# Kernel optimization log

Hardware: AMD Instinct MI355X
Metric: run time of the kernel (lower is better)

Reference implementation:

```python
import jax, jax.numpy as jnp
import numpy as np

T, B, L, I, H = 1024, 1024, 10, 10, 10


def setup_inputs() -> dict:
    key = jax.random.key(0)
    ks = jax.random.split(key, 7)
    scale = 1.0 / np.sqrt(H)
    x = jax.random.normal(ks[0], (T, B, I), dtype=jnp.float32)
    hp = jax.random.normal(ks[1], (L, B, H), dtype=jnp.float32)
    cp = jax.random.normal(ks[2], (L, B, H), dtype=jnp.float32)
    # torch nn.LSTM params, uniform(-1/sqrt(H), 1/sqrt(H)); layer 0 input = I == H so all layers stack
    W_ih = jax.random.uniform(ks[3], (L, 4 * H, I), minval=-scale, maxval=scale, dtype=jnp.float32)
    W_hh = jax.random.uniform(ks[4], (L, 4 * H, H), minval=-scale, maxval=scale, dtype=jnp.float32)
    b_ih = jax.random.uniform(ks[5], (L, 4 * H), minval=-scale, maxval=scale, dtype=jnp.float32)
    b_hh = jax.random.uniform(ks[6], (L, 4 * H), minval=-scale, maxval=scale, dtype=jnp.float32)
    return {"x": x, "hp": hp, "cp": cp, "W_ih": W_ih, "W_hh": W_hh, "b_ih": b_ih, "b_hh": b_hh}


def _run_layer(inp, h0, c0, Wi, Wh, bi, bh):
    # precompute input projections for all timesteps: [T, B, 4H]
    xg = jnp.einsum('tbi,gi->tbg', inp, Wi) + bi + bh

    def step(carry, xg_t):
        h, c = carry
        g = xg_t + h @ Wh.T  # [B, 4H]; torch gate order: i, f, g, o
        i_g, f_g, g_g, o_g = jnp.split(g, 4, axis=-1)
        i_g = jax.nn.sigmoid(i_g)
        f_g = jax.nn.sigmoid(f_g)
        g_g = jnp.tanh(g_g)
        o_g = jax.nn.sigmoid(o_g)
        c = f_g * c + i_g * g_g
        h = o_g * jnp.tanh(c)
        return (h, c), h

    (hT, cT), ys = jax.lax.scan(step, (h0, c0), xg)
    return ys, hT, cT


def reference(x, hp, cp, W_ih, W_hh, b_ih, b_hh):
    out = x
    hns, cns = [], []
    for l in range(hp.shape[0]):  # fixed small layer stack
        out, hn, cn = _run_layer(out, hp[l], cp[l], W_ih[l], W_hh[l], b_ih[l], b_hh[l])
        hns.append(hn)
        cns.append(cn)
    return out, jnp.stack(hns), jnp.stack(cns)
```

## Files before the change

kernel.cpp:

```cpp
#include <hip/hip_runtime.h>

namespace {

constexpr int T = 1024;
constexpr int B = 1024;
constexpr int L = 10;
constexpr int H = 10;
constexpr int NTHREADS = 128;
constexpr int U = 4;
constexpr int NWIN = T / U;
constexpr int NINT = NWIN + L - 1;
constexpr int BH = B * H;
constexpr int WSLOT = 84;

using v2f = __attribute__((ext_vector_type(2))) float;

__device__ __forceinline__ v2f v2fma(v2f a, v2f b, v2f c) {
    return __builtin_elementwise_fma(a, b, c);
}
__device__ __forceinline__ void pin2(v2f& v) { asm volatile("" : "+v"(v)); }
__device__ __forceinline__ void pin1(float& v) { asm volatile("" : "+v"(v)); }

__device__ __forceinline__ float sigmoid_f(float x) {
    return __builtin_amdgcn_rcpf(1.0f + __expf(-x));
}
__device__ __forceinline__ float tanh_f(float x) {
    return 1.0f - 2.0f * __builtin_amdgcn_rcpf(1.0f + __expf(2.0f * x));
}

__global__
__attribute__((amdgpu_flat_work_group_size(NTHREADS, NTHREADS)))
__attribute__((amdgpu_waves_per_eu(1)))
void lstm_pipeline(const float* __restrict__ x,
                   const float* __restrict__ hp,
                   const float* __restrict__ cp,
                   const float* __restrict__ Wih,
                   const float* __restrict__ Whh,
                   const float* __restrict__ bih,
                   const float* __restrict__ bhh,
                   float* __restrict__ out,
                   float* __restrict__ hn,
                   float* __restrict__ cn)
{
    __shared__ __align__(16) float wlds[L * H * WSLOT];
    __shared__ __align__(16) float buf[L + 1][2][U][12];
    __shared__ __align__(16) float hbuf[L][12];

    const int tid = threadIdx.x;
    const int wv = tid >> 6, ln = tid & 63;
    int lidx;
    if (wv == 0) lidx = (ln < 60) ? ln : (ln - 10);
    else         lidx = (ln < 40) ? (60 + ln) : (90 + (ln - 40) % 10);
    const int l = lidx / 10;
    const int j = lidx % 10;
    const int b = blockIdx.x;
    const int boff = b * H + j;

    {
        float* slot = &wlds[lidx * WSLOT];
        #pragma unroll
        for (int g = 0; g < 4; ++g) {
            const int row = l * 4 * H + g * H + j;
            const float* wr = Wih + (size_t)row * H;
            const float* hr = Whh + (size_t)row * H;
            #pragma unroll
            for (int i = 0; i < H; ++i) slot[g * H + i] = wr[i];
            #pragma unroll
            for (int i = 0; i < H; ++i) slot[40 + g * H + i] = hr[i];
            slot[80 + g] = bih[row] + bhh[row];
        }
    }
    __syncthreads();

    v2f wi2[4][5], wh2[4][5];
    float bias[4];
    {
        const float* slot = &wlds[lidx * WSLOT];
        #pragma unroll
        for (int g = 0; g < 4; ++g) {
            #pragma unroll
            for (int p = 0; p < 5; ++p) {
                wi2[g][p] = *(const v2f*)&slot[g * H + 2 * p];
                wh2[g][p] = *(const v2f*)&slot[40 + g * H + 2 * p];
            }
            bias[g] = slot[80 + g];
        }
    }
    #pragma unroll
    for (int g = 0; g < 4; ++g) {
        #pragma unroll
        for (int p = 0; p < 5; ++p) { pin2(wi2[g][p]); pin2(wh2[g][p]); }
        pin1(bias[g]);
    }

    float h = hp[(l * B + b) * H + j];
    float c = cp[(l * B + b) * H + j];
    hbuf[l][j] = h;

    float xcur[U], xnext[U];
    if (lidx < 10) {
        #pragma unroll
        for (int u = 0; u < U; ++u) buf[0][1][u][j] = x[(size_t)u * BH + boff];
        #pragma unroll
        for (int u = 0; u < U; ++u) xcur[u] = x[(size_t)(U + u) * BH + boff];
    }
    __syncthreads();

    auto interval = [&](int k, int wp, int rp) {
        if (lidx < 10 && (k + 2) < NWIN) {
            #pragma unroll
            for (int u = 0; u < U; ++u)
                xnext[u] = x[(size_t)((k + 2) * U + u) * BH + boff];
        }
        const unsigned w = (unsigned)(k - l);
        if (w < (unsigned)NWIN) {
            float hv[U];
            #pragma unroll
            for (int u = 0; u < U; ++u) {
                float xin[10], hin[10];
                {
                    const float* xr = &buf[l][rp][u][0];
                    *(float4*)&xin[0] = *(const float4*)(xr);
                    *(float4*)&xin[4] = *(const float4*)(xr + 4);
                    *(float2*)&xin[8] = *(const float2*)(xr + 8);
                    const float* hr = &hbuf[l][0];
                    *(float4*)&hin[0] = *(const float4*)(hr);
                    *(float4*)&hin[4] = *(const float4*)(hr + 4);
                    *(float2*)&hin[8] = *(const float2*)(hr + 8);
                }
                v2f a0, a1, a2, a3;
                a0[0] = bias[0]; a0[1] = 0.0f;
                a1[0] = bias[1]; a1[1] = 0.0f;
                a2[0] = bias[2]; a2[1] = 0.0f;
                a3[0] = bias[3]; a3[1] = 0.0f;
                #pragma unroll
                for (int p = 0; p < 5; ++p) {
                    v2f xp; xp[0] = xin[2 * p]; xp[1] = xin[2 * p + 1];
                    a0 = v2fma(wi2[0][p], xp, a0);
                    a1 = v2fma(wi2[1][p], xp, a1);
                    a2 = v2fma(wi2[2][p], xp, a2);
                    a3 = v2fma(wi2[3][p], xp, a3);
                }
                #pragma unroll
                for (int p = 0; p < 5; ++p) {
                    v2f hh; hh[0] = hin[2 * p]; hh[1] = hin[2 * p + 1];
                    a0 = v2fma(wh2[0][p], hh, a0);
                    a1 = v2fma(wh2[1][p], hh, a1);
                    a2 = v2fma(wh2[2][p], hh, a2);
                    a3 = v2fma(wh2[3][p], hh, a3);
                }
                const float ig = sigmoid_f(a0[0] + a0[1]);
                const float fg = sigmoid_f(a1[0] + a1[1]);
                const float gg = tanh_f(a2[0] + a2[1]);
                const float og = sigmoid_f(a3[0] + a3[1]);
                c = fmaf(fg, c, ig * gg);
                h = og * tanh_f(c);

                hbuf[l][j] = h;
                buf[l + 1][wp][u][j] = h;
                hv[u] = h;
            }
            if (l == L - 1) {
                const int t0 = (int)w * U;
                #pragma unroll
                for (int u = 0; u < U; ++u)
                    out[(size_t)(t0 + u) * BH + boff] = hv[u];
            }
        }
        if (lidx < 10 && (k + 1) < NWIN) {
            #pragma unroll
            for (int u = 0; u < U; ++u) buf[0][wp][u][j] = xcur[u];
            #pragma unroll
            for (int u = 0; u < U; ++u) xcur[u] = xnext[u];
        }
        __syncthreads();
    };

    for (int kk = 0; kk < NINT + 1; kk += 2) {
        interval(kk, 0, 1);
        interval(kk + 1, 1, 0);
    }

    hn[(l * B + b) * H + j] = h;
    cn[(l * B + b) * H + j] = c;
}

}

extern "C" void kernel_launch(void* const* d_in, const int* in_sizes, int n_in,
                              void* d_out, int out_size, void* d_ws, size_t ws_size,
                              hipStream_t stream) {
    (void)in_sizes; (void)n_in; (void)d_ws; (void)ws_size; (void)out_size;
    const float* x   = (const float*)d_in[0];
    const float* hp  = (const float*)d_in[1];
    const float* cp  = (const float*)d_in[2];
    const float* Wih = (const float*)d_in[3];
    const float* Whh = (const float*)d_in[4];
    const float* bih = (const float*)d_in[5];
    const float* bhh = (const float*)d_in[6];

    float* out = (float*)d_out;
    float* hn  = out + (size_t)T * B * H;
    float* cn  = hn + (size_t)L * B * H;

    lstm_pipeline<<<dim3(B), dim3(NTHREADS), 0, stream>>>(
        x, hp, cp, Wih, Whh, bih, bhh, out, hn, cn);
}
```

Baseline: 502.6 us.

## Split each LSTM hidden unit's gates across two lanes with DPP exchange

Each hidden unit now runs on a pair of lanes, and each lane computes two of the four gates, so the block grows to 256 threads. Inputs and hidden states are stored duplicated, which lets packed v2f FMAs consume them directly, and the four gate activations are exchanged between paired lanes with a DPP swap. The input projection for all U steps is hoisted ahead of the serial recurrence, and the LDS weight staging is replaced by direct global loads. The aim is to halve the per-lane FMA and transcendental work on the critical serial path. The cost is more waves per block, duplicated LDS writes, and a cross-lane shuffle on every step.

New measurement: 638.7 us. 1.27x slower.

```diff
diff --git a/kernel.cpp b/kernel.cpp
--- a/kernel.cpp
+++ b/kernel.cpp
@@ -6,31 +6,30 @@
 constexpr int B = 1024;
 constexpr int L = 10;
 constexpr int H = 10;
-constexpr int NTHREADS = 128;
+constexpr int NTHREADS = 256;
 constexpr int U = 4;
 constexpr int NWIN = T / U;
 constexpr int NINT = NWIN + L - 1;
 constexpr int BH = B * H;
-constexpr int WSLOT = 84;
+constexpr int ROW = 24;
 
 using v2f = __attribute__((ext_vector_type(2))) float;
+using v4f = __attribute__((ext_vector_type(4))) float;
 
 __device__ __forceinline__ v2f v2fma(v2f a, v2f b, v2f c) {
     return __builtin_elementwise_fma(a, b, c);
 }
 __device__ __forceinline__ void pin2(v2f& v) { asm volatile("" : "+v"(v)); }
-__device__ __forceinline__ void pin1(float& v) { asm volatile("" : "+v"(v)); }
-
-__device__ __forceinline__ float sigmoid_f(float x) {
-    return __builtin_amdgcn_rcpf(1.0f + __expf(-x));
-}
-__device__ __forceinline__ float tanh_f(float x) {
-    return 1.0f - 2.0f * __builtin_amdgcn_rcpf(1.0f + __expf(2.0f * x));
-}
+__device__ __forceinline__ float rcp_f(float x) { return __builtin_amdgcn_rcpf(x); }
+__device__ __forceinline__ float dpp_swap1(float v) {
+    return __int_as_float(__builtin_amdgcn_mov_dpp(__float_as_int(v), 0xB1, 0xF, 0xF, true));
+}
+__device__ __forceinline__ v2f lo2(v4f q) { return __builtin_shufflevector(q, q, 0, 1); }
+__device__ __forceinline__ v2f hi2(v4f q) { return __builtin_shufflevector(q, q, 2, 3); }
 
 __global__
 __attribute__((amdgpu_flat_work_group_size(NTHREADS, NTHREADS)))
-__attribute__((amdgpu_waves_per_eu(1)))
+__attribute__((amdgpu_waves_per_eu(4)))
 void lstm_pipeline(const float* __restrict__ x,
                    const float* __restrict__ hp,
                    const float* __restrict__ cp,
@@ -42,136 +41,139 @@
                    float* __restrict__ hn,
                    float* __restrict__ cn)
 {
-    __shared__ __align__(16) float wlds[L * H * WSLOT];
-    __shared__ __align__(16) float buf[L + 1][2][U][12];
-    __shared__ __align__(16) float hbuf[L][12];
+    __shared__ __align__(16) float buf[2][U][L + 1][ROW];
+    __shared__ __align__(16) float hbuf[L][ROW];
 
     const int tid = threadIdx.x;
-    const int wv = tid >> 6, ln = tid & 63;
-    int lidx;
-    if (wv == 0) lidx = (ln < 60) ? ln : (ln - 10);
-    else         lidx = (ln < 40) ? (60 + ln) : (90 + (ln - 40) % 10);
-    const int l = lidx / 10;
-    const int j = lidx % 10;
+    const int wv = tid >> 6;
+    const int ln = tid & 63;
+    int q, l;
+    if (wv < 3) { q = (ln < 60) ? ln : (ln - 8); l = 3 * wv + q / 20; }
+    else        { q = ln % 20;  l = 9; }
+    const int j = (q % 20) >> 1;
+    const int p = q & 1;
     const int b = blockIdx.x;
     const int boff = b * H + j;
 
+    v2f wipk[10], whpk[10], biasv;
     {
-        float* slot = &wlds[lidx * WSLOT];
+        const int r0 = (l * 4 + 2 * p) * H + j;
+        const float* wi0 = Wih + (size_t)r0 * H;
+        const float* wh0 = Whh + (size_t)r0 * H;
         #pragma unroll
-        for (int g = 0; g < 4; ++g) {
-            const int row = l * 4 * H + g * H + j;
-            const float* wr = Wih + (size_t)row * H;
-            const float* hr = Whh + (size_t)row * H;
-            #pragma unroll
-            for (int i = 0; i < H; ++i) slot[g * H + i] = wr[i];
-            #pragma unroll
-            for (int i = 0; i < H; ++i) slot[40 + g * H + i] = hr[i];
-            slot[80 + g] = bih[row] + bhh[row];
-        }
-    }
-    __syncthreads();
-
-    v2f wi2[4][5], wh2[4][5];
-    float bias[4];
-    {
-        const float* slot = &wlds[lidx * WSLOT];
-        #pragma unroll
-        for (int g = 0; g < 4; ++g) {
-            #pragma unroll
-            for (int p = 0; p < 5; ++p) {
-                wi2[g][p] = *(const v2f*)&slot[g * H + 2 * p];
-                wh2[g][p] = *(const v2f*)&slot[40 + g * H + 2 * p];
-            }
-            bias[g] = slot[80 + g];
-        }
+        for (int i = 0; i < H; ++i) {
+            wipk[i][0] = wi0[i]; wipk[i][1] = wi0[H * H + i];
+            whpk[i][0] = wh0[i]; whpk[i][1] = wh0[H * H + i];
+        }
+        biasv[0] = bih[r0] + bhh[r0];
+        biasv[1] = bih[r0 + H] + bhh[r0 + H];
     }
     #pragma unroll
-    for (int g = 0; g < 4; ++g) {
-        #pragma unroll
-        for (int p = 0; p < 5; ++p) { pin2(wi2[g][p]); pin2(wh2[g][p]); }
-        pin1(bias[g]);
-    }
+    for (int i = 0; i < H; ++i) { pin2(wipk[i]); pin2(whpk[i]); }
+    pin2(biasv);
+    const float s0 = p ? 2.0f : -1.0f;
 
     float h = hp[(l * B + b) * H + j];
     float c = cp[(l * B + b) * H + j];
-    hbuf[l][j] = h;
-
-    float xcur[U], xnext[U];
-    if (lidx < 10) {
+    { v2f hh; hh[0] = h; hh[1] = h; *(v2f*)&hbuf[l][2 * j] = hh; }
+
+    const bool stager = (l == 0 && p == 0);
+    float xcur[U];
+    if (stager) {
         #pragma unroll
-        for (int u = 0; u < U; ++u) buf[0][1][u][j] = x[(size_t)u * BH + boff];
+        for (int u = 0; u < U; ++u) {
+            float xv = x[(size_t)u * BH + boff];
+            v2f xx; xx[0] = xv; xx[1] = xv;
+            *(v2f*)&buf[1][u][0][2 * j] = xx;
+        }
         #pragma unroll
         for (int u = 0; u < U; ++u) xcur[u] = x[(size_t)(U + u) * BH + boff];
     }
     __syncthreads();
 
     auto interval = [&](int k, int wp, int rp) {
-        if (lidx < 10 && (k + 2) < NWIN) {
-            #pragma unroll
-            for (int u = 0; u < U; ++u)
-                xnext[u] = x[(size_t)((k + 2) * U + u) * BH + boff];
-        }
         const unsigned w = (unsigned)(k - l);
         if (w < (unsigned)NWIN) {
+            v2f acc[U];
+            #pragma unroll
+            for (int u = 0; u < U; ++u) {
+                const float* xr = &buf[rp][u][l][0];
+                v4f q0 = *(const v4f*)(xr + 0);
+                v4f q1 = *(const v4f*)(xr + 4);
+                v4f q2 = *(const v4f*)(xr + 8);
+                v4f q3 = *(const v4f*)(xr + 12);
+                v4f q4 = *(const v4f*)(xr + 16);
+                v2f z; z[0] = 0.0f; z[1] = 0.0f;
+                v2f a  = v2fma(wipk[0], lo2(q0), biasv);
+                v2f a2 = v2fma(wipk[1], hi2(q0), z);
+                a  = v2fma(wipk[2], lo2(q1), a);
+                a2 = v2fma(wipk[3], hi2(q1), a2);
+                a  = v2fma(wipk[4], lo2(q2), a);
+                a2 = v2fma(wipk[5], hi2(q2), a2);
+                a  = v2fma(wipk[6], lo2(q3), a);
+                a2 = v2fma(wipk[7], hi2(q3), a2);
+                a  = v2fma(wipk[8], lo2(q4), a);
+                a2 = v2fma(wipk[9], hi2(q4), a2);
+                acc[u] = a + a2;
+            }
             float hv[U];
             #pragma unroll
             for (int u = 0; u < U; ++u) {
-                float xin[10], hin[10];
-                {
-                    const float* xr = &buf[l][rp][u][0];
-                    *(float4*)&xin[0] = *(const float4*)(xr);
-                    *(float4*)&xin[4] = *(const float4*)(xr + 4);
-                    *(float2*)&xin[8] = *(const float2*)(xr + 8);
-                    const float* hr = &hbuf[l][0];
-                    *(float4*)&hin[0] = *(const float4*)(hr);
-                    *(float4*)&hin[4] = *(const float4*)(hr + 4);
-                    *(float2*)&hin[8] = *(const float2*)(hr + 8);
-                }
-                v2f a0, a1, a2, a3;
-                a0[0] = bias[0]; a0[1] = 0.0f;
-                a1[0] = bias[1]; a1[1] = 0.0f;
-                a2[0] = bias[2]; a2[1] = 0.0f;
-                a3[0] = bias[3]; a3[1] = 0.0f;
-                #pragma unroll
-                for (int p = 0; p < 5; ++p) {
-                    v2f xp; xp[0] = xin[2 * p]; xp[1] = xin[2 * p + 1];
-                    a0 = v2fma(wi2[0][p], xp, a0);
-                    a1 = v2fma(wi2[1][p], xp, a1);
-                    a2 = v2fma(wi2[2][p], xp, a2);
-                    a3 = v2fma(wi2[3][p], xp, a3);
-                }
-                #pragma unroll
-                for (int p = 0; p < 5; ++p) {
-                    v2f hh; hh[0] = hin[2 * p]; hh[1] = hin[2 * p + 1];
-                    a0 = v2fma(wh2[0][p], hh, a0);
-                    a1 = v2fma(wh2[1][p], hh, a1);
-                    a2 = v2fma(wh2[2][p], hh, a2);
-                    a3 = v2fma(wh2[3][p], hh, a3);
-                }
-                const float ig = sigmoid_f(a0[0] + a0[1]);
-                const float fg = sigmoid_f(a1[0] + a1[1]);
-                const float gg = tanh_f(a2[0] + a2[1]);
-                const float og = sigmoid_f(a3[0] + a3[1]);
+                const float* hr = &hbuf[l][0];
+                v4f q0 = *(const v4f*)(hr + 0);
+                v4f q1 = *(const v4f*)(hr + 4);
+                v4f q2 = *(const v4f*)(hr + 8);
+                v4f q3 = *(const v4f*)(hr + 12);
+                v4f q4 = *(const v4f*)(hr + 16);
+                v2f z; z[0] = 0.0f; z[1] = 0.0f;
+                v2f a  = v2fma(whpk[0], lo2(q0), acc[u]);
+                v2f a2 = v2fma(whpk[1], hi2(q0), z);
+                a  = v2fma(whpk[2], lo2(q1), a);
+                a2 = v2fma(whpk[3], hi2(q1), a2);
+                a  = v2fma(whpk[4], lo2(q2), a);
+                a2 = v2fma(whpk[5], hi2(q2), a2);
+                a  = v2fma(whpk[6], lo2(q3), a);
+                a2 = v2fma(whpk[7], hi2(q3), a2);
+                a  = v2fma(whpk[8], lo2(q4), a);
+                a2 = v2fma(whpk[9], hi2(q4), a2);
+                v2f pre = a + a2;
+                const float e0 = __expf(pre[0] * s0);
+                const float e1 = __expf(-pre[1]);
+                const float r0 = rcp_f(1.0f + e0);
+                const float r1 = rcp_f(1.0f + e1);
+                const float x0 = dpp_swap1(r0);
+                const float x1 = dpp_swap1(r1);
+                const float ig = p ? x0 : r0;
+                const float fg = p ? x1 : r1;
+                const float og = p ? r1 : x1;
+                const float gs = p ? r0 : x0;
+                const float gg = fmaf(-2.0f, gs, 1.0f);
                 c = fmaf(fg, c, ig * gg);
-                h = og * tanh_f(c);
-
-                hbuf[l][j] = h;
-                buf[l + 1][wp][u][j] = h;
+                const float th = 1.0f - 2.0f * rcp_f(1.0f + __expf(2.0f * c));
+                h = og * th;
+                v2f hh; hh[0] = h; hh[1] = h;
+                *(v2f*)&hbuf[l][2 * j] = hh;
+                *(v2f*)&buf[wp][u][l + 1][2 * j] = hh;
                 hv[u] = h;
             }
-            if (l == L - 1) {
+            if (l == L - 1 && p == 0) {
                 const int t0 = (int)w * U;
                 #pragma unroll
                 for (int u = 0; u < U; ++u)
                     out[(size_t)(t0 + u) * BH + boff] = hv[u];
             }
         }
-        if (lidx < 10 && (k + 1) < NWIN) {
+        if (stager && (k + 1) < NWIN) {
             #pragma unroll
-            for (int u = 0; u < U; ++u) buf[0][wp][u][j] = xcur[u];
-            #pragma unroll
-            for (int u = 0; u < U; ++u) xcur[u] = xnext[u];
+            for (int u = 0; u < U; ++u) {
+                v2f xx; xx[0] = xcur[u]; xx[1] = xcur[u];
+                *(v2f*)&buf[wp][u][0][2 * j] = xx;
+            }
+            if ((k + 2) < NWIN) {
+                #pragma unroll
+                for (int u = 0; u < U; ++u)
+                    xcur[u] = x[(size_t)((k + 2) * U + u) * BH + boff];
+            }
         }
         __syncthreads();
     };
```

## Process two batch rows per block with gate-paired packed FMAs and hoisted input projections

Applied to the files above, without the earlier changes.

Each block now handles two batch rows, so every thread's register-resident weights are reused across both rows and the grid is halved. Weights are repacked so each packed FMA computes two gates at once with duplicated inputs stored in LDS. The input projection for all U substeps is hoisted ahead of the recurrent chain. The exp and rcp calls of the two rows are interleaved to expose instruction-level parallelism. This trades fewer blocks (512 on a 256-CU part) and doubled per-block serial work for more ILP and fewer redundant weight loads and syncs.

New measurement: 834.1 us. +66.0%, slower.

```diff
diff --git a/kernel.cpp b/kernel.cpp
--- a/kernel.cpp
+++ b/kernel.cpp
@@ -7,26 +7,23 @@
 constexpr int L = 10;
 constexpr int H = 10;
 constexpr int NTHREADS = 128;
+constexpr int NB = 2;
 constexpr int U = 4;
 constexpr int NWIN = T / U;
 constexpr int NINT = NWIN + L - 1;
 constexpr int BH = B * H;
-constexpr int WSLOT = 84;
+constexpr int ROWF = 20;
 
 using v2f = __attribute__((ext_vector_type(2))) float;
+using v4f = __attribute__((ext_vector_type(4))) float;
 
 __device__ __forceinline__ v2f v2fma(v2f a, v2f b, v2f c) {
     return __builtin_elementwise_fma(a, b, c);
 }
 __device__ __forceinline__ void pin2(v2f& v) { asm volatile("" : "+v"(v)); }
-__device__ __forceinline__ void pin1(float& v) { asm volatile("" : "+v"(v)); }
-
-__device__ __forceinline__ float sigmoid_f(float x) {
-    return __builtin_amdgcn_rcpf(1.0f + __expf(-x));
-}
-__device__ __forceinline__ float tanh_f(float x) {
-    return 1.0f - 2.0f * __builtin_amdgcn_rcpf(1.0f + __expf(2.0f * x));
-}
+__device__ __forceinline__ float rcp_f(float x) { return __builtin_amdgcn_rcpf(x); }
+__device__ __forceinline__ v2f lo2(v4f q) { return __builtin_shufflevector(q, q, 0, 1); }
+__device__ __forceinline__ v2f hi2(v4f q) { return __builtin_shufflevector(q, q, 2, 3); }
 
 __global__
 __attribute__((amdgpu_flat_work_group_size(NTHREADS, NTHREADS)))
@@ -42,134 +39,174 @@
                    float* __restrict__ hn,
                    float* __restrict__ cn)
 {
-    __shared__ __align__(16) float wlds[L * H * WSLOT];
-    __shared__ __align__(16) float buf[L + 1][2][U][12];
-    __shared__ __align__(16) float hbuf[L][12];
+    __shared__ __align__(16) float buf[NB][2][U][L + 1][ROWF];
 
     const int tid = threadIdx.x;
-    const int wv = tid >> 6, ln = tid & 63;
+    const int wv = tid >> 6;
+    const int ln = tid & 63;
     int lidx;
     if (wv == 0) lidx = (ln < 60) ? ln : (ln - 10);
     else         lidx = (ln < 40) ? (60 + ln) : (90 + (ln - 40) % 10);
     const int l = lidx / 10;
     const int j = lidx % 10;
-    const int b = blockIdx.x;
-    const int boff = b * H + j;
-
+    const int bbase = blockIdx.x * NB;
+
+    const bool is_st = (wv == 0) ? (ln < 10) : (ln >= 40 && ln < 50);
+    const int stb = wv;
+    const int stj = (wv == 0) ? ln : (ln - 40);
+    const int stboff = (bbase + stb) * H + stj;
+
+    v2f wiA[10], wiB[10], whA[10], whB[10], bA, bB;
     {
-        float* slot = &wlds[lidx * WSLOT];
+        const float* WiL = Wih + (size_t)l * 4 * H * H;
+        const float* WhL = Whh + (size_t)l * 4 * H * H;
         #pragma unroll
-        for (int g = 0; g < 4; ++g) {
-            const int row = l * 4 * H + g * H + j;
-            const float* wr = Wih + (size_t)row * H;
-            const float* hr = Whh + (size_t)row * H;
-            #pragma unroll
-            for (int i = 0; i < H; ++i) slot[g * H + i] = wr[i];
-            #pragma unroll
-            for (int i = 0; i < H; ++i) slot[40 + g * H + i] = hr[i];
-            slot[80 + g] = bih[row] + bhh[row];
-        }
+        for (int k = 0; k < 10; ++k) {
+            wiA[k][0] = WiL[(0 * H + j) * H + k]; wiA[k][1] = WiL[(1 * H + j) * H + k];
+            wiB[k][0] = WiL[(2 * H + j) * H + k]; wiB[k][1] = WiL[(3 * H + j) * H + k];
+            whA[k][0] = WhL[(0 * H + j) * H + k]; whA[k][1] = WhL[(1 * H + j) * H + k];
+            whB[k][0] = WhL[(2 * H + j) * H + k]; whB[k][1] = WhL[(3 * H + j) * H + k];
+        }
+        const int bo = l * 4 * H;
+        bA[0] = bih[bo + j] + bhh[bo + j];
+        bA[1] = bih[bo + H + j] + bhh[bo + H + j];
+        bB[0] = bih[bo + 2 * H + j] + bhh[bo + 2 * H + j];
+        bB[1] = bih[bo + 3 * H + j] + bhh[bo + 3 * H + j];
+    }
+    #pragma unroll
+    for (int k = 0; k < 10; ++k) { pin2(wiA[k]); pin2(wiB[k]); pin2(whA[k]); pin2(whB[k]); }
+    pin2(bA); pin2(bB);
+
+    float hs[NB], cs[NB];
+    #pragma unroll
+    for (int bb = 0; bb < NB; ++bb) {
+        hs[bb] = hp[((size_t)l * B + bbase + bb) * H + j];
+        cs[bb] = cp[((size_t)l * B + bbase + bb) * H + j];
+        v2f hh; hh[0] = hs[bb]; hh[1] = hs[bb];
+        *(v2f*)&buf[bb][0][U - 1][l + 1][2 * j] = hh;
+        *(v2f*)&buf[bb][1][U - 1][l + 1][2 * j] = hh;
+    }
+
+    float xcur[U], xnext[U];
+    if (is_st) {
+        #pragma unroll
+        for (int u = 0; u < U; ++u) {
+            float xv = x[(size_t)u * BH + stboff];
+            v2f xx; xx[0] = xv; xx[1] = xv;
+            *(v2f*)&buf[stb][1][u][0][2 * stj] = xx;
+        }
+        #pragma unroll
+        for (int u = 0; u < U; ++u) xcur[u] = x[(size_t)(U + u) * BH + stboff];
     }
     __syncthreads();
 
-    v2f wi2[4][5], wh2[4][5];
-    float bias[4];
-    {
-        const float* slot = &wlds[lidx * WSLOT];
-        #pragma unroll
-        for (int g = 0; g < 4; ++g) {
-            #pragma unroll
-            for (int p = 0; p < 5; ++p) {
-                wi2[g][p] = *(const v2f*)&slot[g * H + 2 * p];
-                wh2[g][p] = *(const v2f*)&slot[40 + g * H + 2 * p];
-            }
-            bias[g] = slot[80 + g];
-        }
-    }
-    #pragma unroll
-    for (int g = 0; g < 4; ++g) {
-        #pragma unroll
-        for (int p = 0; p < 5; ++p) { pin2(wi2[g][p]); pin2(wh2[g][p]); }
-        pin1(bias[g]);
-    }
-
-    float h = hp[(l * B + b) * H + j];
-    float c = cp[(l * B + b) * H + j];
-    hbuf[l][j] = h;
-
-    float xcur[U], xnext[U];
-    if (lidx < 10) {
-        #pragma unroll
-        for (int u = 0; u < U; ++u) buf[0][1][u][j] = x[(size_t)u * BH + boff];
-        #pragma unroll
-        for (int u = 0; u < U; ++u) xcur[u] = x[(size_t)(U + u) * BH + boff];
-    }
-    __syncthreads();
-
     auto interval = [&](int k, int wp, int rp) {
-        if (lidx < 10 && (k + 2) < NWIN) {
+        if (is_st && (k + 2) < NWIN) {
             #pragma unroll
             for (int u = 0; u < U; ++u)
-                xnext[u] = x[(size_t)((k + 2) * U + u) * BH + boff];
+                xnext[u] = x[(size_t)((k + 2) * U + u) * BH + stboff];
         }
         const unsigned w = (unsigned)(k - l);
         if (w < (unsigned)NWIN) {
-            float hv[U];
+            v2f aA[NB][U], aB[NB][U];
+            #pragma unroll
+            for (int bb = 0; bb < NB; ++bb) {
+                #pragma unroll
+                for (int u = 0; u < U; ++u) {
+                    const float* xr = &buf[bb][rp][u][l][0];
+                    v4f q0 = *(const v4f*)(xr + 0);
+                    v4f q1 = *(const v4f*)(xr + 4);
+                    v4f q2 = *(const v4f*)(xr + 8);
+                    v4f q3 = *(const v4f*)(xr + 12);
+                    v4f q4 = *(const v4f*)(xr + 16);
+                    v2f a  = v2fma(wiA[0], lo2(q0), bA);
+                    v2f bv = v2fma(wiB[0], lo2(q0), bB);
+                    a = v2fma(wiA[1], hi2(q0), a);  bv = v2fma(wiB[1], hi2(q0), bv);
+                    a = v2fma(wiA[2], lo2(q1), a);  bv = v2fma(wiB[2], lo2(q1), bv);
+                    a = v2fma(wiA[3], hi2(q1), a);  bv = v2fma(wiB[3], hi2(q1), bv);
+                    a = v2fma(wiA[4], lo2(q2), a);  bv = v2fma(wiB[4], lo2(q2), bv);
+                    a = v2fma(wiA[5], hi2(q2), a);  bv = v2fma(wiB[5], hi2(q2), bv);
+                    a = v2fma(wiA[6], lo2(q3), a);  bv = v2fma(wiB[6], lo2(q3), bv);
+                    a = v2fma(wiA[7], hi2(q3), a);  bv = v2fma(wiB[7], hi2(q3), bv);
+                    a = v2fma(wiA[8], lo2(q4), a);  bv = v2fma(wiB[8], lo2(q4), bv);
+                    a = v2fma(wiA[9], hi2(q4), a);  bv = v2fma(wiB[9], hi2(q4), bv);
+                    aA[bb][u] = a; aB[bb][u] = bv;
+                }
+            }
+            float hv[NB][U];
             #pragma unroll
             for (int u = 0; u < U; ++u) {
-                float xin[10], hin[10];
-                {
-                    const float* xr = &buf[l][rp][u][0];
-                    *(float4*)&xin[0] = *(const float4*)(xr);
-                    *(float4*)&xin[4] = *(const float4*)(xr + 4);
-                    *(float2*)&xin[8] = *(const float2*)(xr + 8);
-                    const float* hr = &hbuf[l][0];
-                    *(float4*)&hin[0] = *(const float4*)(hr);
-                    *(float4*)&hin[4] = *(const float4*)(hr + 4);
-                    *(float2*)&hin[8] = *(const float2*)(hr + 8);
-                }
-                v2f a0, a1, a2, a3;
-                a0[0] = bias[0]; a0[1] = 0.0f;
-                a1[0] = bias[1]; a1[1] = 0.0f;
-                a2[0] = bias[2]; a2[1] = 0.0f;
-                a3[0] = bias[3]; a3[1] = 0.0f;
-                #pragma unroll
-                for (int p = 0; p < 5; ++p) {
-                    v2f xp; xp[0] = xin[2 * p]; xp[1] = xin[2 * p + 1];
-                    a0 = v2fma(wi2[0][p], xp, a0);
-                    a1 = v2fma(wi2[1][p], xp, a1);
-                    a2 = v2fma(wi2[2][p], xp, a2);
-                    a3 = v2fma(wi2[3][p], xp, a3);
-                }
-                #pragma unroll
-                for (int p = 0; p < 5; ++p) {
-                    v2f hh; hh[0] = hin[2 * p]; hh[1] = hin[2 * p + 1];
-                    a0 = v2fma(wh2[0][p], hh, a0);
-                    a1 = v2fma(wh2[1][p], hh, a1);
-                    a2 = v2fma(wh2[2][p], hh, a2);
-                    a3 = v2fma(wh2[3][p], hh, a3);
-                }
-                const float ig = sigmoid_f(a0[0] + a0[1]);
-                const float fg = sigmoid_f(a1[0] + a1[1]);
-                const float gg = tanh_f(a2[0] + a2[1]);
-                const float og = sigmoid_f(a3[0] + a3[1]);
-                c = fmaf(fg, c, ig * gg);
-                h = og * tanh_f(c);
-
-                hbuf[l][j] = h;
-                buf[l + 1][wp][u][j] = h;
-                hv[u] = h;
+                v2f pA[NB], pB[NB];
+                #pragma unroll
+                for (int bb = 0; bb < NB; ++bb) {
+                    const float* hr = (u == 0) ? &buf[bb][rp][U - 1][l + 1][0]
+                                               : &buf[bb][wp][u - 1][l + 1][0];
+                    v4f q0 = *(const v4f*)(hr + 0);
+                    v4f q1 = *(const v4f*)(hr + 4);
+                    v4f q2 = *(const v4f*)(hr + 8);
+                    v4f q3 = *(const v4f*)(hr + 12);
+                    v4f q4 = *(const v4f*)(hr + 16);
+                    v2f a  = v2fma(whA[0], lo2(q0), aA[bb][u]);
+                    v2f bv = v2fma(whB[0], lo2(q0), aB[bb][u]);
+                    a = v2fma(whA[1], hi2(q0), a);  bv = v2fma(whB[1], hi2(q0), bv);
+                    a = v2fma(whA[2], lo2(q1), a);  bv = v2fma(whB[2], lo2(q1), bv);
+                    a = v2fma(whA[3], hi2(q1), a);  bv = v2fma(whB[3], hi2(q1), bv);
+                    a = v2fma(whA[4], lo2(q2), a);  bv = v2fma(whB[4], lo2(q2), bv);
+                    a = v2fma(whA[5], hi2(q2), a);  bv = v2fma(whB[5], hi2(q2), bv);
+                    a = v2fma(whA[6], lo2(q3), a);  bv = v2fma(whB[6], lo2(q3), bv);
+                    a = v2fma(whA[7], hi2(q3), a);  bv = v2fma(whB[7], hi2(q3), bv);
+                    a = v2fma(whA[8], lo2(q4), a);  bv = v2fma(whB[8], lo2(q4), bv);
+                    a = v2fma(whA[9], hi2(q4), a);  bv = v2fma(whB[9], hi2(q4), bv);
+                    pA[bb] = a; pB[bb] = bv;
+                }
+                float ei[NB], ef[NB], eg[NB], eo[NB];
+                #pragma unroll
+                for (int bb = 0; bb < NB; ++bb) {
+                    ei[bb] = __expf(-pA[bb][0]);
+                    ef[bb] = __expf(-pA[bb][1]);
+                    eg[bb] = __expf(2.0f * pB[bb][0]);
+                    eo[bb] = __expf(-pB[bb][1]);
+                }
+                float ig[NB], fg[NB], gr[NB], og[NB];
+                #pragma unroll
+                for (int bb = 0; bb < NB; ++bb) {
+                    ig[bb] = rcp_f(1.0f + ei[bb]);
+                    fg[bb] = rcp_f(1.0f + ef[bb]);
+                    gr[bb] = rcp_f(1.0f + eg[bb]);
+                    og[bb] = rcp_f(1.0f + eo[bb]);
+                }
+                float et[NB];
+                #pragma unroll
+                for (int bb = 0; bb < NB; ++bb) {
+                    const float gg = 1.0f - 2.0f * gr[bb];
+                    cs[bb] = fmaf(fg[bb], cs[bb], ig[bb] * gg);
+                    et[bb] = __expf(2.0f * cs[bb]);
+                }
+                #pragma unroll
+                for (int bb = 0; bb < NB; ++bb) {
+                    const float th = 1.0f - 2.0f * rcp_f(1.0f + et[bb]);
+                    const float h = og[bb] * th;
+                    hs[bb] = h;
+                    v2f hh; hh[0] = h; hh[1] = h;
+                    *(v2f*)&buf[bb][wp][u][l + 1][2 * j] = hh;
+                    hv[bb][u] = h;
+                }
             }
             if (l == L - 1) {
                 const int t0 = (int)w * U;
                 #pragma unroll
-                for (int u = 0; u < U; ++u)
-                    out[(size_t)(t0 + u) * BH + boff] = hv[u];
-            }
-        }
-        if (lidx < 10 && (k + 1) < NWIN) {
-            #pragma unroll
-            for (int u = 0; u < U; ++u) buf[0][wp][u][j] = xcur[u];
+                for (int bb = 0; bb < NB; ++bb)
+                    #pragma unroll
+                    for (int u = 0; u < U; ++u)
+                        out[(size_t)(t0 + u) * BH + (bbase + bb) * H + j] = hv[bb][u];
+            }
+        }
+        if (is_st && (k + 1) < NWIN) {
+            #pragma unroll
+            for (int u = 0; u < U; ++u) {
+                v2f xx; xx[0] = xcur[u]; xx[1] = xcur[u];
+                *(v2f*)&buf[stb][wp][u][0][2 * stj] = xx;
+            }
             #pragma unroll
             for (int u = 0; u < U; ++u) xcur[u] = xnext[u];
         }
@@ -181,8 +218,11 @@
         interval(kk + 1, 1, 0);
     }
 
-    hn[(l * B + b) * H + j] = h;
-    cn[(l * B + b) * H + j] = c;
+    #pragma unroll
+    for (int bb = 0; bb < NB; ++bb) {
+        hn[((size_t)l * B + bbase + bb) * H + j] = hs[bb];
+        cn[((size_t)l * B + bbase + bb) * H + j] = cs[bb];
+    }
 }
 
 }
@@ -203,6 +243,6 @@
     float* hn  = out + (size_t)T * B * H;
     float* cn  = hn + (size_t)L * B * H;
 
-    lstm_pipeline<<<dim3(B), dim3(NTHREADS), 0, stream>>>(
+    lstm_pipeline<<<dim3(B / NB), dim3(NTHREADS), 0, stream>>>(
         x, hp, cp, Wih, Whh, bih, bhh, out, hn, cn);
 }
```
